# Optimization experiments

Hardware: AMD Instinct MI355X
Metric: run time of the kernel (lower is better)

The kernel has to match this reference:

```python
import jax, jax.numpy as jnp
import numpy as np

EPS = 1e-5

def conv1d(x, w, b, pad):
    # x: [B,C_in,S], w: [C_out,C_in,K] -> [B,C_out,S]
    y = jax.lax.conv_general_dilated(x, w, window_strides=(1,), padding=[(pad, pad)],
                                     dimension_numbers=('NCH', 'OIH', 'NCH'))
    return y + b[None, :, None]

def bn(x, gamma, beta, mean, var):
    # inference-mode BatchNorm1d over channel dim of [B,C,S]
    scale = gamma * jax.lax.rsqrt(var + EPS)
    shift = beta - mean * scale
    return x * scale[None, :, None] + shift[None, :, None]

def setup_inputs() -> dict:
    key = jax.random.key(0)
    ks = jax.random.split(key, 16)
    B, S, D, C, K = 32, 2048, 128, 256, 5
    x = jax.random.normal(ks[0], (B, S, D), dtype=jnp.float32)
    start_padding_indices = jax.random.randint(ks[1], (B,), 0, S, dtype=jnp.int64 if jax.config.jax_enable_x64 else jnp.int32)
    def conv_init(k, co, ci, kk):
        fan = ci * kk
        return jax.random.normal(k, (co, ci, kk), dtype=jnp.float32) / np.sqrt(fan)
    W1 = conv_init(ks[2], C, D, K); b1 = jnp.zeros((C,), jnp.float32)
    g1 = jnp.ones((C,), jnp.float32); be1 = jnp.zeros((C,), jnp.float32)
    m1 = jax.random.normal(ks[3], (C,), dtype=jnp.float32) * 0.1
    v1 = jax.random.uniform(ks[4], (C,), dtype=jnp.float32, minval=0.5, maxval=1.5)
    W2 = conv_init(ks[5], C, C, K); b2 = jnp.zeros((C,), jnp.float32)
    g2 = jnp.ones((C,), jnp.float32); be2 = jnp.zeros((C,), jnp.float32)
    m2 = jax.random.normal(ks[6], (C,), dtype=jnp.float32) * 0.1
    v2 = jax.random.uniform(ks[7], (C,), dtype=jnp.float32, minval=0.5, maxval=1.5)
    Wf = conv_init(ks[8], D, C, 1); bf = jnp.zeros((D,), jnp.float32)
    return {"x": x, "start_padding_indices": start_padding_indices,
            "W1": W1, "b1": b1, "g1": g1, "be1": be1, "m1": m1, "v1": v1,
            "W2": W2, "b2": b2, "g2": g2, "be2": be2, "m2": m2, "v2": v2,
            "Wf": Wf, "bf": bf}

def reference(x, start_padding_indices, W1, b1, g1, be1, m1, v1,
              W2, b2, g2, be2, m2, v2, Wf, bf):
    B, S, D = x.shape
    K = W1.shape[-1]
    h = jnp.transpose(x, (0, 2, 1))                      # [B,D,S]
    h = jax.nn.relu(bn(conv1d(h, W1, b1, K // 2), g1, be1, m1, v1))
    h = jax.nn.relu(bn(conv1d(h, W2, b2, K // 2), g2, be2, m2, v2))
    h = conv1d(h, Wf, bf, 0)                             # [B,D,S]
    conv_out = jnp.transpose(h, (0, 2, 1))               # [B,S,D]
    # vectorized masked mean: -1 sentinel -> full length; 0 -> zeros
    lengths = jnp.where(start_padding_indices == -1, S, start_padding_indices)  # [B]
    mask = jnp.arange(S)[None, :] < lengths[:, None]     # [B,S]
    sums = jnp.sum(conv_out * mask[:, :, None].astype(conv_out.dtype), axis=1)  # [B,D]
    denom = jnp.maximum(lengths, 1).astype(conv_out.dtype)[:, None]
    pooled = jnp.where(lengths[:, None] > 0, sums / denom, jnp.zeros_like(sums))
    return pooled
```

## Files before the change

### kernel.cpp

```cpp
#include <hip/hip_runtime.h>

#define S_LEN 2048
#define NBATCH 32

typedef __bf16 bf16x8 __attribute__((ext_vector_type(8)));
typedef float f32x4 __attribute__((ext_vector_type(4)));
typedef unsigned short bf_t;

__device__ __forceinline__ unsigned short f2bf(float f) {
  __bf16 h = (__bf16)f;
  return __builtin_bit_cast(unsigned short, h);
}

#if __has_builtin(__builtin_amdgcn_global_load_lds)
#define USE_GLL 1
#else
#define USE_GLL 0
#endif

__device__ __forceinline__ void load_lds16(const void* g, void* ldsbase) {
#if USE_GLL
  __builtin_amdgcn_global_load_lds(
      (const __attribute__((address_space(1))) unsigned int*)g,
      (__attribute__((address_space(3))) unsigned int*)ldsbase, 16, 0, 0);
#endif
}

__global__ void convert_x(const float* __restrict__ x, bf_t* __restrict__ xb) {
  const size_t i = (size_t)blockIdx.x * blockDim.x + threadIdx.x;
  const float4 a = ((const float4*)x)[2 * i];
  const float4 c = ((const float4*)x)[2 * i + 1];
  ushort4 o0; o0.x = f2bf(a.x); o0.y = f2bf(a.y); o0.z = f2bf(a.z); o0.w = f2bf(a.w);
  ushort4 o1; o1.x = f2bf(c.x); o1.y = f2bf(c.y); o1.z = f2bf(c.z); o1.w = f2bf(c.w);
  ((ushort4*)xb)[2 * i] = o0;
  ((ushort4*)xb)[2 * i + 1] = o1;
}

__global__ void fold_bn(const float* __restrict__ b1, const float* __restrict__ g1,
                        const float* __restrict__ be1, const float* __restrict__ m1,
                        const float* __restrict__ v1,
                        const float* __restrict__ b2, const float* __restrict__ g2,
                        const float* __restrict__ be2, const float* __restrict__ m2,
                        const float* __restrict__ v2, float* __restrict__ abuf) {
  int c = threadIdx.x;
  if (c < 256) {
    float a1 = g1[c] * rsqrtf(v1[c] + 1e-5f);
    abuf[c] = a1;
    abuf[256 + c] = (b1[c] - m1[c]) * a1 + be1[c];
    float a2 = g2[c] * rsqrtf(v2[c] + 1e-5f);
    abuf[512 + c] = a2;
    abuf[768 + c] = (b2[c] - m2[c]) * a2 + be2[c];
  }
}

template <int CIN, int TAPS>
__global__ void prep_w2(const float* __restrict__ w, bf_t* __restrict__ wfm) {
  const int idx = blockIdx.x * 256 + threadIdx.x;
  constexpr int total = 256 * CIN * TAPS;
  if (idx >= total) return;
  const int j = idx & 7;
  const int l = (idx >> 3) & 63;
  const int f = (idx >> 9) & 7;
  const int wr = (idx >> 12) & 1;
  const int tg = idx >> 13;
  const int co = wr * 128 + f * 16 + (l & 15);
  const int cc = tg / (TAPS * 4);
  const int k = (tg / 4) % TAPS;
  const int q = tg & 3;
  const int ci = cc * 128 + q * 32 + (l >> 4) * 8 + j;
  wfm[idx] = f2bf(w[((size_t)co * CIN + ci) * TAPS + k]);
}

template <int CIN, int COUT, int TAPS>
__global__ void prep_w(const float* __restrict__ w, bf_t* __restrict__ wfm) {
  constexpr int T = CIN * TAPS / 32;
  const int idx = blockIdx.x * 256 + threadIdx.x;
  constexpr int total = COUT * CIN * TAPS;
  if (idx >= total) return;
  const int j = idx & 7;
  const int l = (idx >> 3) & 63;
  const int f = (idx >> 9) & 3;
  const int gt = idx >> 11;
  const int t = gt % T;
  const int g = gt / T;
  const int co = g * 64 + f * 16 + (l & 15);
  const int cc = t / (TAPS * 4);
  const int k = (t / 4) % TAPS;
  const int q = t & 3;
  const int ci = cc * 128 + q * 32 + (l >> 4) * 8 + j;
  wfm[idx] = f2bf(w[((size_t)co * CIN + ci) * TAPS + k]);
}

template <int CIN, int TAPS>
__global__ __launch_bounds__(512, 2)
void conv_bn_relu(const bf_t* __restrict__ xin, const bf_t* __restrict__ wfm,
                  const float* __restrict__ alpha, const float* __restrict__ bias,
                  bf_t* __restrict__ hout) {
  constexpr int CC = CIN / 128;
  constexpr int HALO = (TAPS - 1) / 2;
  constexpr int NROWS = 256 + 2 * HALO;
  constexpr int TCC = TAPS * 4;
  constexpr int P = CC * TCC / 2;
  constexpr int XSL = NROWS * 256;

  __shared__ char smem[65536 + XSL];
  char* xsm = smem + 65536;

  const int tid = threadIdx.x;
  const int l = tid & 63;
  const int wv = tid >> 6;
  const int wr = wv >> 2;
  const int wn = wv & 3;
  const int b = blockIdx.x >> 3;
  const int s0 = (blockIdx.x & 7) << 8;
  const int l15 = l & 15;
  const int l4 = l >> 4;

  f32x4 acc[8][4] = {};

  auto STAGE_A = [&](int pg) {
    const char* srcw = (const char*)wfm + (size_t)pg * 32768;
    char* ab = smem + (pg & 1) * 32768;
#pragma unroll
    for (int it = 0; it < 4; ++it) {
      const int off = tid * 16 + it * 8192;
#if USE_GLL
      load_lds16(srcw + off, ab + (off - l * 16));
#else
      *(int4*)(ab + off) = *(const int4*)(srcw + off);
#endif
    }
  };

  auto STAGE_X = [&](int cc) {
    const char* src = (const char*)xin + ((size_t)b * S_LEN * CIN + cc * 128) * 2;
    for (int off = tid * 16; off < XSL; off += 512 * 16) {
      const int row = off >> 8;
      const int c = off & 255;
      const int s = s0 - HALO + row;
      const int cs = c ^ ((row & 7) << 4);
      void* lb = (void*)(xsm + (off - l * 16));
      if ((unsigned)s < (unsigned)S_LEN) {
#if USE_GLL
        load_lds16(src + (size_t)s * (CIN * 2) + cs, lb);
#else
        *(int4*)(xsm + off) = *(const int4*)(src + (size_t)s * (CIN * 2) + cs);
#endif
      } else {
        *(int4*)(xsm + off) = make_int4(0, 0, 0, 0);
      }
    }
  };

  STAGE_X(0);
  STAGE_A(0);

#pragma unroll 1
  for (int p = 0; p < P; ++p) {
    __syncthreads();
    const int cc = p / (TCC / 2);
    const int kk = p % (TCC / 2);
    if (CC > 1 && p > 0 && kk == 0) {
      STAGE_X(cc);
      __syncthreads();
    }
    if (p + 1 < P) STAGE_A(p + 1);
    const char* ab = smem + (p & 1) * 32768 + wr * 8192;

#pragma unroll
    for (int j2 = 0; j2 < 2; ++j2) {
      const int t = kk * 2 + j2;
      const int k = t >> 2;
      const int q = t & 3;
      bf16x8 bfr[4];
#pragma unroll
      for (int fn = 0; fn < 4; ++fn) {
        const int row = wn * 64 + fn * 16 + l15 + k;
        const int cb = q * 64 + l4 * 16;
        bfr[fn] = *(const bf16x8*)(xsm + row * 256 + (cb ^ ((row & 7) << 4)));
      }
#pragma unroll
      for (int f = 0; f < 8; ++f) {
        const bf16x8 afr = *(const bf16x8*)(ab + j2 * 16384 + f * 1024 + l * 16);
#pragma unroll
        for (int n = 0; n < 4; ++n)
          acc[f][n] = __builtin_amdgcn_mfma_f32_16x16x32_bf16(
              afr, bfr[n], acc[f][n], 0, 0, 0);
      }
    }
  }

  const int cobase = wr * 128;
#pragma unroll
  for (int f = 0; f < 8; ++f) {
    const int co0 = cobase + f * 16 + l4 * 4;
    const f32x4 al = *(const f32x4*)(alpha + co0);
    const f32x4 bi = *(const f32x4*)(bias + co0);
#pragma unroll
    for (int n = 0; n < 4; ++n) {
      const int s = s0 + wn * 64 + n * 16 + l15;
      ushort4 pk;
      pk.x = f2bf(fmaxf(acc[f][n][0] * al[0] + bi[0], 0.f));
      pk.y = f2bf(fmaxf(acc[f][n][1] * al[1] + bi[1], 0.f));
      pk.z = f2bf(fmaxf(acc[f][n][2] * al[2] + bi[2], 0.f));
      pk.w = f2bf(fmaxf(acc[f][n][3] * al[3] + bi[3], 0.f));
      *(ushort4*)((char*)hout + ((size_t)(b * S_LEN + s) * 256 + co0) * 2) = pk;
    }
  }
}

__global__ __launch_bounds__(512, 4)
void conv_pool(const bf_t* __restrict__ xin, const bf_t* __restrict__ wfm,
               const float* __restrict__ bfin, const int* __restrict__ spi,
               float* __restrict__ gpart) {
  constexpr int CIN = 256;
  constexpr int T = 8;

  __shared__ char smem[128 * 256];
  __shared__ float red[4][128];

  const int tid = threadIdx.x;
  const int l = tid & 63;
  const int wv = tid >> 6;
  const int wr = wv >> 2;
  const int wn = wv & 3;
  const int nb = blockIdx.x;
  const int b = nb >> 4;
  const int st = nb & 15;
  const int s0 = st << 7;
  const int l15 = l & 15;
  const int l4 = l >> 4;

  f32x4 acc[4][2] = {};
  const bf_t* wbase = wfm + (size_t)wr * (T * 2048);

  for (int cc = 0; cc < 2; ++cc) {
    const char* src = (const char*)xin + ((size_t)b * S_LEN * CIN + cc * 128) * 2;
    for (int off = tid * 16; off < 128 * 256; off += 512 * 16) {
      const int row = off >> 8;
      const int c = off & 255;
      const int cs = c ^ ((row & 7) << 4);
      void* ldsbase = (void*)(smem + (off - l * 16));
#if USE_GLL
      load_lds16(src + (size_t)(s0 + row) * (CIN * 2) + cs, ldsbase);
#else
      *(int4*)(smem + off) = *(const int4*)(src + (size_t)(s0 + row) * (CIN * 2) + cs);
#endif
    }
    __syncthreads();

#pragma unroll
    for (int q = 0; q < 4; ++q) {
      const int t = cc * 4 + q;
      bf16x8 bfr[2];
#pragma unroll
      for (int fn = 0; fn < 2; ++fn) {
        const int row = wn * 32 + fn * 16 + l15;
        const int cb = q * 64 + l4 * 16;
        bfr[fn] = *(const bf16x8*)(smem + row * 256 + (cb ^ ((row & 7) << 4)));
      }
#pragma unroll
      for (int f = 0; f < 4; ++f) {
        const bf16x8 afr =
            *(const bf16x8*)(wbase + ((size_t)(t * 4 + f) * 64 + l) * 8);
        acc[f][0] = __builtin_amdgcn_mfma_f32_16x16x32_bf16(afr, bfr[0], acc[f][0], 0, 0, 0);
        acc[f][1] = __builtin_amdgcn_mfma_f32_16x16x32_bf16(afr, bfr[1], acc[f][1], 0, 0, 0);
      }
    }
    __syncthreads();
  }

  int len = spi[b];
  if (len < 0) len = S_LEN;

#pragma unroll
  for (int f = 0; f < 4; ++f) {
    const int co0 = wr * 64 + f * 16 + l4 * 4;
    const f32x4 bi = *(const f32x4*)(bfin + co0);
    f32x4 vs = {};
#pragma unroll
    for (int fn = 0; fn < 2; ++fn) {
      const int s = s0 + wn * 32 + fn * 16 + l15;
      const float m = (s < len) ? 1.f : 0.f;
      vs[0] += (acc[f][fn][0] + bi[0]) * m;
      vs[1] += (acc[f][fn][1] + bi[1]) * m;
      vs[2] += (acc[f][fn][2] + bi[2]) * m;
      vs[3] += (acc[f][fn][3] + bi[3]) * m;
    }
#pragma unroll
    for (int d = 1; d < 16; d <<= 1) {
      vs[0] += __shfl_xor(vs[0], d, 64);
      vs[1] += __shfl_xor(vs[1], d, 64);
      vs[2] += __shfl_xor(vs[2], d, 64);
      vs[3] += __shfl_xor(vs[3], d, 64);
    }
    if (l15 == 0) {
      red[wn][co0 + 0] = vs[0];
      red[wn][co0 + 1] = vs[1];
      red[wn][co0 + 2] = vs[2];
      red[wn][co0 + 3] = vs[3];
    }
  }
  __syncthreads();
  if (tid < 128) {
    float p = red[0][tid] + red[1][tid] + red[2][tid] + red[3][tid];
    gpart[((size_t)b * 16 + st) * 128 + tid] = p;
  }
}

__global__ void finalize(const float* __restrict__ gpart, const int* __restrict__ spi,
                         float* __restrict__ out) {
  const int b = blockIdx.x;
  const int d = threadIdx.x;
  float s = 0.f;
#pragma unroll
  for (int t = 0; t < 16; ++t) s += gpart[((size_t)b * 16 + t) * 128 + d];
  int len = spi[b];
  if (len < 0) len = S_LEN;
  float denom = (float)(len < 1 ? 1 : len);
  out[b * 128 + d] = s / denom;
}

extern "C" void kernel_launch(void* const* d_in, const int* in_sizes, int n_in,
                              void* d_out, int out_size, void* d_ws, size_t ws_size,
                              hipStream_t stream) {
  (void)in_sizes; (void)n_in; (void)out_size; (void)ws_size;
  const float* x = (const float*)d_in[0];
  const int* spi = (const int*)d_in[1];
  const float* W1 = (const float*)d_in[2];
  const float* b1 = (const float*)d_in[3];
  const float* g1 = (const float*)d_in[4];
  const float* be1 = (const float*)d_in[5];
  const float* m1 = (const float*)d_in[6];
  const float* v1 = (const float*)d_in[7];
  const float* W2 = (const float*)d_in[8];
  const float* b2 = (const float*)d_in[9];
  const float* g2 = (const float*)d_in[10];
  const float* be2 = (const float*)d_in[11];
  const float* m2 = (const float*)d_in[12];
  const float* v2 = (const float*)d_in[13];
  const float* Wf = (const float*)d_in[14];
  const float* bf_ = (const float*)d_in[15];
  float* out = (float*)d_out;

  char* ws = (char*)d_ws;
  bf_t* xb   = (bf_t*)(ws);
  bf_t* h1   = (bf_t*)(ws + 16777216);
  bf_t* h2   = (bf_t*)(ws + 50331648);
  bf_t* wf1  = (bf_t*)(ws + 83886080);
  bf_t* wf2  = (bf_t*)(ws + 84213760);
  bf_t* wff  = (bf_t*)(ws + 84869120);
  float* abuf  = (float*)(ws + 84934656);
  float* gpart = (float*)(ws + 84938752);

  convert_x<<<4096, 256, 0, stream>>>(x, xb);
  fold_bn<<<1, 256, 0, stream>>>(b1, g1, be1, m1, v1, b2, g2, be2, m2, v2, abuf);
  prep_w2<128, 5><<<640, 256, 0, stream>>>(W1, wf1);
  prep_w2<256, 5><<<1280, 256, 0, stream>>>(W2, wf2);
  prep_w<256, 128, 1><<<128, 256, 0, stream>>>(Wf, wff);

  conv_bn_relu<128, 5><<<256, 512, 0, stream>>>(xb, wf1, abuf, abuf + 256, h1);
  conv_bn_relu<256, 5><<<256, 512, 0, stream>>>(h1, wf2, abuf + 512, abuf + 768, h2);
  conv_pool<<<512, 512, 0, stream>>>(h2, wff, bf_, spi, gpart);
  finalize<<<32, 128, 0, stream>>>(gpart, spi, out);
}
```

Measured before the change: 106.8 us.

## Fuse fp32 input conversion into conv1 staging and deepen weight pipeline to four buffers

Removes the separate convert_x kernel. The first conv now reads fp32 x directly and converts it to bf16 while staging into LDS, which saves a full write and re-read of the bf16 copy of the input. The weight staging loop changes from double-buffered 32KB stages to a four-slot ring of 16KB stages with three loads in flight. Explicit vmcnt/lgkmcnt waits and raw s_barrier replace __syncthreads. The hand-written wait counts are fragile and could cause races if the outstanding-load accounting is off, and the fp32 staging uses plain loads rather than direct-to-LDS loads.

```diff
diff --git a/kernel.cpp b/kernel.cpp
--- a/kernel.cpp
+++ b/kernel.cpp
@@ -24,16 +24,6 @@
       (const __attribute__((address_space(1))) unsigned int*)g,
       (__attribute__((address_space(3))) unsigned int*)ldsbase, 16, 0, 0);
 #endif
-}
-
-__global__ void convert_x(const float* __restrict__ x, bf_t* __restrict__ xb) {
-  const size_t i = (size_t)blockIdx.x * blockDim.x + threadIdx.x;
-  const float4 a = ((const float4*)x)[2 * i];
-  const float4 c = ((const float4*)x)[2 * i + 1];
-  ushort4 o0; o0.x = f2bf(a.x); o0.y = f2bf(a.y); o0.z = f2bf(a.z); o0.w = f2bf(a.w);
-  ushort4 o1; o1.x = f2bf(c.x); o1.y = f2bf(c.y); o1.z = f2bf(c.z); o1.w = f2bf(c.w);
-  ((ushort4*)xb)[2 * i] = o0;
-  ((ushort4*)xb)[2 * i + 1] = o1;
 }
 
 __global__ void fold_bn(const float* __restrict__ b1, const float* __restrict__ g1,
@@ -91,16 +81,16 @@
   wfm[idx] = f2bf(w[((size_t)co * CIN + ci) * TAPS + k]);
 }
 
-template <int CIN, int TAPS>
+template <int CIN, int TAPS, bool F32IN>
 __global__ __launch_bounds__(512, 2)
-void conv_bn_relu(const bf_t* __restrict__ xin, const bf_t* __restrict__ wfm,
+void conv_bn_relu(const void* __restrict__ xin, const bf_t* __restrict__ wfm,
                   const float* __restrict__ alpha, const float* __restrict__ bias,
                   bf_t* __restrict__ hout) {
   constexpr int CC = CIN / 128;
   constexpr int HALO = (TAPS - 1) / 2;
   constexpr int NROWS = 256 + 2 * HALO;
   constexpr int TCC = TAPS * 4;
-  constexpr int P = CC * TCC / 2;
+  constexpr int P = CC * TCC;
   constexpr int XSL = NROWS * 256;
 
   __shared__ char smem[65536 + XSL];
@@ -118,11 +108,11 @@
 
   f32x4 acc[8][4] = {};
 
-  auto STAGE_A = [&](int pg) {
-    const char* srcw = (const char*)wfm + (size_t)pg * 32768;
-    char* ab = smem + (pg & 1) * 32768;
-#pragma unroll
-    for (int it = 0; it < 4; ++it) {
+  auto STAGE_A = [&](int t) {
+    const char* srcw = (const char*)wfm + (size_t)t * 16384;
+    char* ab = smem + (t & 3) * 16384;
+#pragma unroll
+    for (int it = 0; it < 2; ++it) {
       const int off = tid * 16 + it * 8192;
 #if USE_GLL
       load_lds16(srcw + off, ab + (off - l * 16));
@@ -132,7 +122,7 @@
     }
   };
 
-  auto STAGE_X = [&](int cc) {
+  auto STAGE_X_BF = [&](int cc) {
     const char* src = (const char*)xin + ((size_t)b * S_LEN * CIN + cc * 128) * 2;
     for (int off = tid * 16; off < XSL; off += 512 * 16) {
       const int row = off >> 8;
@@ -152,41 +142,65 @@
     }
   };
 
-  STAGE_X(0);
-  STAGE_A(0);
+  auto STAGE_X_F32 = [&]() {
+    const float* xf = (const float*)xin + (size_t)b * S_LEN * 128;
+    for (int off = tid * 16; off < XSL; off += 512 * 16) {
+      const int row = off >> 8;
+      const int c = off & 255;
+      const int s = s0 - HALO + row;
+      const int cs = c ^ ((row & 7) << 4);
+      int4 v = make_int4(0, 0, 0, 0);
+      if ((unsigned)s < (unsigned)S_LEN) {
+        const float4 a = *(const float4*)(xf + (size_t)s * 128 + (c >> 1));
+        const float4 d = *(const float4*)(xf + (size_t)s * 128 + (c >> 1) + 4);
+        v.x = (int)((unsigned)f2bf(a.x) | ((unsigned)f2bf(a.y) << 16));
+        v.y = (int)((unsigned)f2bf(a.z) | ((unsigned)f2bf(a.w) << 16));
+        v.z = (int)((unsigned)f2bf(d.x) | ((unsigned)f2bf(d.y) << 16));
+        v.w = (int)((unsigned)f2bf(d.z) | ((unsigned)f2bf(d.w) << 16));
+      }
+      *(int4*)(xsm + row * 256 + cs) = v;
+    }
+  };
+
+  if constexpr (F32IN) STAGE_X_F32(); else STAGE_X_BF(0);
+  STAGE_A(0); STAGE_A(1); STAGE_A(2);
+  asm volatile("s_waitcnt lgkmcnt(0)" ::: "memory");
 
 #pragma unroll 1
   for (int p = 0; p < P; ++p) {
-    __syncthreads();
-    const int cc = p / (TCC / 2);
-    const int kk = p % (TCC / 2);
-    if (CC > 1 && p > 0 && kk == 0) {
-      STAGE_X(cc);
-      __syncthreads();
-    }
-    if (p + 1 < P) STAGE_A(p + 1);
-    const char* ab = smem + (p & 1) * 32768 + wr * 8192;
-
-#pragma unroll
-    for (int j2 = 0; j2 < 2; ++j2) {
-      const int t = kk * 2 + j2;
-      const int k = t >> 2;
-      const int q = t & 3;
-      bf16x8 bfr[4];
-#pragma unroll
-      for (int fn = 0; fn < 4; ++fn) {
-        const int row = wn * 64 + fn * 16 + l15 + k;
-        const int cb = q * 64 + l4 * 16;
-        bfr[fn] = *(const bf16x8*)(xsm + row * 256 + (cb ^ ((row & 7) << 4)));
-      }
-#pragma unroll
-      for (int f = 0; f < 8; ++f) {
-        const bf16x8 afr = *(const bf16x8*)(ab + j2 * 16384 + f * 1024 + l * 16);
-#pragma unroll
-        for (int n = 0; n < 4; ++n)
-          acc[f][n] = __builtin_amdgcn_mfma_f32_16x16x32_bf16(
-              afr, bfr[n], acc[f][n], 0, 0, 0);
-      }
+    if (p < P - 2)       asm volatile("s_waitcnt vmcnt(4) lgkmcnt(0)" ::: "memory");
+    else if (p == P - 2) asm volatile("s_waitcnt vmcnt(2) lgkmcnt(0)" ::: "memory");
+    else                 asm volatile("s_waitcnt vmcnt(0) lgkmcnt(0)" ::: "memory");
+    __builtin_amdgcn_s_barrier();
+    __builtin_amdgcn_sched_barrier(0);
+
+    if (CC > 1 && p == TCC) {
+      STAGE_X_BF(1);
+      asm volatile("s_waitcnt vmcnt(0) lgkmcnt(0)" ::: "memory");
+      __builtin_amdgcn_s_barrier();
+      __builtin_amdgcn_sched_barrier(0);
+    }
+    if (p + 3 < P) STAGE_A(p + 3);
+
+    const int tt = (CC > 1) ? (p % TCC) : p;
+    const int k = tt >> 2;
+    const int q = tt & 3;
+    const char* ab = smem + (p & 3) * 16384 + wr * 8192;
+
+    bf16x8 bfr[4];
+#pragma unroll
+    for (int fn = 0; fn < 4; ++fn) {
+      const int row = wn * 64 + fn * 16 + l15 + k;
+      const int cb = q * 64 + l4 * 16;
+      bfr[fn] = *(const bf16x8*)(xsm + row * 256 + (cb ^ ((row & 7) << 4)));
+    }
+#pragma unroll
+    for (int f = 0; f < 8; ++f) {
+      const bf16x8 afr = *(const bf16x8*)(ab + f * 1024 + l * 16);
+#pragma unroll
+      for (int n = 0; n < 4; ++n)
+        acc[f][n] = __builtin_amdgcn_mfma_f32_16x16x32_bf16(
+            afr, bfr[n], acc[f][n], 0, 0, 0);
     }
   }
 
@@ -344,7 +358,6 @@
   float* out = (float*)d_out;
 
   char* ws = (char*)d_ws;
-  bf_t* xb   = (bf_t*)(ws);
   bf_t* h1   = (bf_t*)(ws + 16777216);
   bf_t* h2   = (bf_t*)(ws + 50331648);
   bf_t* wf1  = (bf_t*)(ws + 83886080);
@@ -353,14 +366,13 @@
   float* abuf  = (float*)(ws + 84934656);
   float* gpart = (float*)(ws + 84938752);
 
-  convert_x<<<4096, 256, 0, stream>>>(x, xb);
   fold_bn<<<1, 256, 0, stream>>>(b1, g1, be1, m1, v1, b2, g2, be2, m2, v2, abuf);
   prep_w2<128, 5><<<640, 256, 0, stream>>>(W1, wf1);
   prep_w2<256, 5><<<1280, 256, 0, stream>>>(W2, wf2);
   prep_w<256, 128, 1><<<128, 256, 0, stream>>>(Wf, wff);
 
-  conv_bn_relu<128, 5><<<256, 512, 0, stream>>>(xb, wf1, abuf, abuf + 256, h1);
-  conv_bn_relu<256, 5><<<256, 512, 0, stream>>>(h1, wf2, abuf + 512, abuf + 768, h2);
+  conv_bn_relu<128, 5, true><<<256, 512, 0, stream>>>(x, wf1, abuf, abuf + 256, h1);
+  conv_bn_relu<256, 5, false><<<256, 512, 0, stream>>>(h1, wf2, abuf + 512, abuf + 768, h2);
   conv_pool<<<512, 512, 0, stream>>>(h2, wff, bf_, spi, gpart);
   finalize<<<32, 128, 0, stream>>>(gpart, spi, out);
 }
```

After: 108.8 us. Within noise of the previous version (+1.9%).

## Pipeline conv GEMM with per-tap B staging and explicit vmcnt waits

Applied to the files above, without the earlier changes.

Restructures the conv+BN+ReLU kernel into a software-pipelined GEMM. Weight (A) and shifted-input (B) tiles are staged per tap via global_load_lds into 128KB of double-buffered LDS, and out-of-range halo rows are redirected to a zero page instead of being written separately. Each k-step is split into four MFMA half-phases, with stage loads issued in between and synchronised through raw s_barrier, explicit vmcnt/lgkmcnt waits and setprio. The goal is to overlap global loads with MFMA and drop the full-halo x slab reloads. The cost is much more LDS, which may reduce occupancy, and fragile hand-counted waits.

```diff
diff --git a/kernel.cpp b/kernel.cpp
--- a/kernel.cpp
+++ b/kernel.cpp
@@ -23,8 +23,17 @@
   __builtin_amdgcn_global_load_lds(
       (const __attribute__((address_space(1))) unsigned int*)g,
       (__attribute__((address_space(3))) unsigned int*)ldsbase, 16, 0, 0);
+#else
+  *(int4*)((char*)ldsbase + (threadIdx.x & 63) * 16) =
+      *(const int4*)((const char*)g);
 #endif
 }
+
+#define WAITV10 asm volatile("s_waitcnt vmcnt(10)" ::: "memory")
+#define WAITV8  asm volatile("s_waitcnt vmcnt(8)" ::: "memory")
+#define WAITV4  asm volatile("s_waitcnt vmcnt(4)" ::: "memory")
+#define WAITV0  asm volatile("s_waitcnt vmcnt(0)" ::: "memory")
+#define LGKM0   asm volatile("s_waitcnt lgkmcnt(0)" ::: "memory")
 
 __global__ void convert_x(const float* __restrict__ x, bf_t* __restrict__ xb) {
   const size_t i = (size_t)blockIdx.x * blockDim.x + threadIdx.x;
@@ -41,8 +50,10 @@
                         const float* __restrict__ v1,
                         const float* __restrict__ b2, const float* __restrict__ g2,
                         const float* __restrict__ be2, const float* __restrict__ m2,
-                        const float* __restrict__ v2, float* __restrict__ abuf) {
+                        const float* __restrict__ v2, float* __restrict__ abuf,
+                        float* __restrict__ zp) {
   int c = threadIdx.x;
+  if (c < 64) zp[c] = 0.f;
   if (c < 256) {
     float a1 = g1[c] * rsqrtf(v1[c] + 1e-5f);
     abuf[c] = a1;
@@ -93,18 +104,14 @@
 
 template <int CIN, int TAPS>
 __global__ __launch_bounds__(512, 2)
-void conv_bn_relu(const bf_t* __restrict__ xin, const bf_t* __restrict__ wfm,
-                  const float* __restrict__ alpha, const float* __restrict__ bias,
-                  bf_t* __restrict__ hout) {
-  constexpr int CC = CIN / 128;
+void conv_gemm(const bf_t* __restrict__ xin, const bf_t* __restrict__ wfm,
+               const float* __restrict__ alpha, const float* __restrict__ bias,
+               const float* __restrict__ zp, bf_t* __restrict__ hout) {
   constexpr int HALO = (TAPS - 1) / 2;
-  constexpr int NROWS = 256 + 2 * HALO;
-  constexpr int TCC = TAPS * 4;
-  constexpr int P = CC * TCC / 2;
-  constexpr int XSL = NROWS * 256;
-
-  __shared__ char smem[65536 + XSL];
-  char* xsm = smem + 65536;
+  constexpr int P = (CIN / 128) * TAPS * 4;
+  constexpr int NKT = P / 2;
+
+  __shared__ char smem[131072];
 
   const int tid = threadIdx.x;
   const int l = tid & 63;
@@ -115,79 +122,114 @@
   const int s0 = (blockIdx.x & 7) << 8;
   const int l15 = l & 15;
   const int l4 = l >> 4;
+  const int wu16 = (tid - l) * 16;
 
   f32x4 acc[8][4] = {};
 
-  auto STAGE_A = [&](int pg) {
-    const char* srcw = (const char*)wfm + (size_t)pg * 32768;
-    char* ab = smem + (pg & 1) * 32768;
-#pragma unroll
-    for (int it = 0; it < 4; ++it) {
-      const int off = tid * 16 + it * 8192;
-#if USE_GLL
-      load_lds16(srcw + off, ab + (off - l * 16));
-#else
-      *(int4*)(ab + off) = *(const int4*)(srcw + off);
-#endif
-    }
+  auto STAGE_A = [&](int t) {
+    const char* src = (const char*)wfm + (size_t)t * 16384;
+    char* dst = smem + ((t >> 1) & 1) * 32768 + (t & 1) * 16384;
+    load_lds16(src + tid * 16, dst + wu16);
+    load_lds16(src + 8192 + tid * 16, dst + 8192 + wu16);
   };
 
-  auto STAGE_X = [&](int cc) {
-    const char* src = (const char*)xin + ((size_t)b * S_LEN * CIN + cc * 128) * 2;
-    for (int off = tid * 16; off < XSL; off += 512 * 16) {
-      const int row = off >> 8;
-      const int c = off & 255;
-      const int s = s0 - HALO + row;
-      const int cs = c ^ ((row & 7) << 4);
-      void* lb = (void*)(xsm + (off - l * 16));
-      if ((unsigned)s < (unsigned)S_LEN) {
-#if USE_GLL
-        load_lds16(src + (size_t)s * (CIN * 2) + cs, lb);
-#else
-        *(int4*)(xsm + off) = *(const int4*)(src + (size_t)s * (CIN * 2) + cs);
-#endif
-      } else {
-        *(int4*)(xsm + off) = make_int4(0, 0, 0, 0);
-      }
+  auto STAGE_B = [&](int j, int sub) {
+    const int t = 2 * j + sub;
+    const int cc = t / (TAPS * 4);
+    const int k = (t >> 2) % TAPS;
+    const int q = t & 3;
+    char* dst = smem + 65536 + (j & 1) * 32768 + sub * 16384;
+    const char* srcb = (const char*)xin +
+        ((size_t)b * S_LEN * CIN + cc * 128 + q * 32) * 2 + (tid & 3) * 16;
+    const int r0 = tid >> 2;
+    {
+      const int s = s0 + r0 - HALO + k;
+      const char* src = ((unsigned)s < (unsigned)S_LEN)
+          ? srcb + (size_t)s * (CIN * 2) : (const char*)zp;
+      load_lds16(src, dst + wu16);
+    }
+    {
+      const int s = s0 + r0 + 128 - HALO + k;
+      const char* src = ((unsigned)s < (unsigned)S_LEN)
+          ? srcb + (size_t)s * (CIN * 2) : (const char*)zp;
+      load_lds16(src, dst + 8192 + wu16);
     }
   };
 
-  STAGE_X(0);
-  STAGE_A(0);
+  STAGE_A(0); STAGE_B(0, 0); STAGE_A(1); STAGE_B(0, 1);
+  STAGE_A(2); STAGE_B(1, 0); STAGE_A(3);
+  WAITV10;
+  __builtin_amdgcn_s_barrier();
 
 #pragma unroll 1
-  for (int p = 0; p < P; ++p) {
-    __syncthreads();
-    const int cc = p / (TCC / 2);
-    const int kk = p % (TCC / 2);
-    if (CC > 1 && p > 0 && kk == 0) {
-      STAGE_X(cc);
-      __syncthreads();
-    }
-    if (p + 1 < P) STAGE_A(p + 1);
-    const char* ab = smem + (p & 1) * 32768 + wr * 8192;
-
-#pragma unroll
-    for (int j2 = 0; j2 < 2; ++j2) {
-      const int t = kk * 2 + j2;
-      const int k = t >> 2;
-      const int q = t & 3;
-      bf16x8 bfr[4];
-#pragma unroll
-      for (int fn = 0; fn < 4; ++fn) {
-        const int row = wn * 64 + fn * 16 + l15 + k;
-        const int cb = q * 64 + l4 * 16;
-        bfr[fn] = *(const bf16x8*)(xsm + row * 256 + (cb ^ ((row & 7) << 4)));
-      }
-#pragma unroll
-      for (int f = 0; f < 8; ++f) {
-        const bf16x8 afr = *(const bf16x8*)(ab + j2 * 16384 + f * 1024 + l * 16);
-#pragma unroll
-        for (int n = 0; n < 4; ++n)
-          acc[f][n] = __builtin_amdgcn_mfma_f32_16x16x32_bf16(
-              afr, bfr[n], acc[f][n], 0, 0, 0);
-      }
-    }
+  for (int j = 0; j < NKT; ++j) {
+    const char* Ab = smem + (j & 1) * 32768;
+    const char* Bb = smem + 65536 + (j & 1) * 32768;
+    bf16x8 afr[8], bfr0, bfr1;
+
+#pragma unroll
+    for (int f = 0; f < 8; ++f)
+      afr[f] = *(const bf16x8*)(Ab + wr * 8192 + f * 1024 + l * 16);
+    bfr0 = *(const bf16x8*)(Bb + (wn * 64 + 0 + l15) * 64 + l4 * 16);
+    bfr1 = *(const bf16x8*)(Bb + (wn * 64 + 16 + l15) * 64 + l4 * 16);
+    if (j + 1 < NKT) STAGE_B(j + 1, 1);
+    __builtin_amdgcn_s_barrier();
+    LGKM0; __builtin_amdgcn_sched_barrier(0);
+    __builtin_amdgcn_s_setprio(1);
+#pragma unroll
+    for (int f = 0; f < 8; ++f) {
+      acc[f][0] = __builtin_amdgcn_mfma_f32_16x16x32_bf16(afr[f], bfr0, acc[f][0], 0, 0, 0);
+      acc[f][1] = __builtin_amdgcn_mfma_f32_16x16x32_bf16(afr[f], bfr1, acc[f][1], 0, 0, 0);
+    }
+    __builtin_amdgcn_s_setprio(0);
+    __builtin_amdgcn_s_barrier();
+
+    bfr0 = *(const bf16x8*)(Bb + (wn * 64 + 32 + l15) * 64 + l4 * 16);
+    bfr1 = *(const bf16x8*)(Bb + (wn * 64 + 48 + l15) * 64 + l4 * 16);
+    if (j + 2 < NKT) STAGE_A(2 * (j + 2));
+    __builtin_amdgcn_s_barrier();
+    LGKM0; __builtin_amdgcn_sched_barrier(0);
+    __builtin_amdgcn_s_setprio(1);
+#pragma unroll
+    for (int f = 0; f < 8; ++f) {
+      acc[f][2] = __builtin_amdgcn_mfma_f32_16x16x32_bf16(afr[f], bfr0, acc[f][2], 0, 0, 0);
+      acc[f][3] = __builtin_amdgcn_mfma_f32_16x16x32_bf16(afr[f], bfr1, acc[f][3], 0, 0, 0);
+    }
+    __builtin_amdgcn_s_setprio(0);
+    if (j <= NKT - 3) { WAITV10; } else if (j == NKT - 2) { WAITV8; } else { WAITV0; }
+    __builtin_amdgcn_s_barrier();
+
+#pragma unroll
+    for (int f = 0; f < 8; ++f)
+      afr[f] = *(const bf16x8*)(Ab + 16384 + wr * 8192 + f * 1024 + l * 16);
+    bfr0 = *(const bf16x8*)(Bb + 16384 + (wn * 64 + 0 + l15) * 64 + l4 * 16);
+    bfr1 = *(const bf16x8*)(Bb + 16384 + (wn * 64 + 16 + l15) * 64 + l4 * 16);
+    if (j + 2 < NKT) STAGE_B(j + 2, 0);
+    __builtin_amdgcn_s_barrier();
+    LGKM0; __builtin_amdgcn_sched_barrier(0);
+    __builtin_amdgcn_s_setprio(1);
+#pragma unroll
+    for (int f = 0; f < 8; ++f) {
+      acc[f][0] = __builtin_amdgcn_mfma_f32_16x16x32_bf16(afr[f], bfr0, acc[f][0], 0, 0, 0);
+      acc[f][1] = __builtin_amdgcn_mfma_f32_16x16x32_bf16(afr[f], bfr1, acc[f][1], 0, 0, 0);
+    }
+    __builtin_amdgcn_s_setprio(0);
+    __builtin_amdgcn_s_barrier();
+
+    bfr0 = *(const bf16x8*)(Bb + 16384 + (wn * 64 + 32 + l15) * 64 + l4 * 16);
+    bfr1 = *(const bf16x8*)(Bb + 16384 + (wn * 64 + 48 + l15) * 64 + l4 * 16);
+    if (j + 2 < NKT) STAGE_A(2 * (j + 2) + 1);
+    __builtin_amdgcn_s_barrier();
+    LGKM0; __builtin_amdgcn_sched_barrier(0);
+    __builtin_amdgcn_s_setprio(1);
+#pragma unroll
+    for (int f = 0; f < 8; ++f) {
+      acc[f][2] = __builtin_amdgcn_mfma_f32_16x16x32_bf16(afr[f], bfr0, acc[f][2], 0, 0, 0);
+      acc[f][3] = __builtin_amdgcn_mfma_f32_16x16x32_bf16(afr[f], bfr1, acc[f][3], 0, 0, 0);
+    }
+    __builtin_amdgcn_s_setprio(0);
+    if (j + 2 < NKT) { WAITV10; } else if (j + 1 < NKT) { WAITV4; }
+    __builtin_amdgcn_s_barrier();
   }
 
   const int cobase = wr * 128;
@@ -241,11 +283,7 @@
       const int c = off & 255;
       const int cs = c ^ ((row & 7) << 4);
       void* ldsbase = (void*)(smem + (off - l * 16));
-#if USE_GLL
       load_lds16(src + (size_t)(s0 + row) * (CIN * 2) + cs, ldsbase);
-#else
-      *(int4*)(smem + off) = *(const int4*)(src + (size_t)(s0 + row) * (CIN * 2) + cs);
-#endif
     }
     __syncthreads();
 
@@ -344,23 +382,24 @@
   float* out = (float*)d_out;
 
   char* ws = (char*)d_ws;
-  bf_t* xb   = (bf_t*)(ws);
-  bf_t* h1   = (bf_t*)(ws + 16777216);
-  bf_t* h2   = (bf_t*)(ws + 50331648);
-  bf_t* wf1  = (bf_t*)(ws + 83886080);
-  bf_t* wf2  = (bf_t*)(ws + 84213760);
-  bf_t* wff  = (bf_t*)(ws + 84869120);
-  float* abuf  = (float*)(ws + 84934656);
-  float* gpart = (float*)(ws + 84938752);
+  float* zp   = (float*)(ws);
+  bf_t* xb    = (bf_t*)(ws + 4096);
+  bf_t* h1    = (bf_t*)(ws + 16781312);
+  bf_t* h2    = (bf_t*)(ws + 50335744);
+  bf_t* wf1   = (bf_t*)(ws + 83890176);
+  bf_t* wf2   = (bf_t*)(ws + 84217856);
+  bf_t* wff   = (bf_t*)(ws + 84873216);
+  float* abuf = (float*)(ws + 84938752);
+  float* gpart= (float*)(ws + 84942848);
 
   convert_x<<<4096, 256, 0, stream>>>(x, xb);
-  fold_bn<<<1, 256, 0, stream>>>(b1, g1, be1, m1, v1, b2, g2, be2, m2, v2, abuf);
+  fold_bn<<<1, 256, 0, stream>>>(b1, g1, be1, m1, v1, b2, g2, be2, m2, v2, abuf, zp);
   prep_w2<128, 5><<<640, 256, 0, stream>>>(W1, wf1);
   prep_w2<256, 5><<<1280, 256, 0, stream>>>(W2, wf2);
   prep_w<256, 128, 1><<<128, 256, 0, stream>>>(Wf, wff);
 
-  conv_bn_relu<128, 5><<<256, 512, 0, stream>>>(xb, wf1, abuf, abuf + 256, h1);
-  conv_bn_relu<256, 5><<<256, 512, 0, stream>>>(h1, wf2, abuf + 512, abuf + 768, h2);
+  conv_gemm<128, 5><<<256, 512, 0, stream>>>(xb, wf1, abuf, abuf + 256, zp, h1);
+  conv_gemm<256, 5><<<256, 512, 0, stream>>>(h1, wf2, abuf + 512, abuf + 768, zp, h2);
   conv_pool<<<512, 512, 0, stream>>>(h2, wff, bf_, spi, gpart);
   finalize<<<32, 128, 0, stream>>>(gpart, spi, out);
 }
```

Result: slower. 113.7 us (+6.5%).
